# Optimization experiments

Measured on AMD Instinct MI355X. Metric: run time of the kernel, lower is better.

Reference implementation:

```python
import jax, jax.numpy as jnp
import numpy as np

B, S, H = 2, 2048, 1024
NH = 16
HD = H // NH
SCALE = 1.0 / np.sqrt(HD).astype(np.float32)


def setup_inputs() -> dict:
    key = jax.random.key(0)
    ks = jax.random.split(key, 7)
    lim = 1.0 / np.sqrt(H)  # lecun-ish init scale for linear weights
    return {
        "query": jax.random.normal(ks[0], (B, S, H), dtype=jnp.float32),
        "key_in": jax.random.normal(ks[1], (B, S, H), dtype=jnp.float32),
        "value": jax.random.normal(ks[2], (B, S, H), dtype=jnp.float32),
        "attention_mask": jnp.ones((B, S), dtype=jnp.int32),
        "Wq": jax.random.uniform(ks[3], (H, H), jnp.float32, -lim, lim),
        "Wk": jax.random.uniform(ks[4], (H, H), jnp.float32, -lim, lim),
        "Wv": jax.random.uniform(ks[5], (H, H), jnp.float32, -lim, lim),
        "Wo": jax.random.uniform(ks[6], (H, H), jnp.float32, -lim, lim),
    }


def reference(query, key_in, value, attention_mask, Wq, Wk, Wv, Wo):
    b, s, _ = query.shape
    # projections (no bias)
    q = (query @ Wq).reshape(b, s, NH, HD).transpose(0, 2, 1, 3)  # [b,h,s,d]
    k = (key_in @ Wk).reshape(b, s, NH, HD).transpose(0, 2, 1, 3)
    v = (value @ Wv).reshape(b, s, NH, HD).transpose(0, 2, 1, 3)

    scores = jnp.einsum("bhqd,bhkd->bhqk", q, k) * SCALE  # [b,h,s,s]
    mask = attention_mask[:, None, None, :]  # broadcast over heads & query pos
    scores = jnp.where(mask == 0, -1e9, scores)
    attn = jax.nn.softmax(scores, axis=-1)

    ctx = jnp.einsum("bhqk,bhkd->bhqd", attn, v)
    ctx = ctx.transpose(0, 2, 1, 3).reshape(b, s, H)
    out = ctx @ Wo
    return out, jnp.mean(attn, axis=1)
```

## Files before the change

kernel.cpp:

```cpp
#include <hip/hip_runtime.h>
#include <stdint.h>

#define BB 2
#define SS 2048
#define HH 1024
#define NHEAD 16
#define HDIM 64

constexpr int   BSROWS = BB * SS;
constexpr float SCALE  = 0.125f;
constexpr float LOG2E  = 1.4426950408889634f;
constexpr float SL     = SCALE * LOG2E;

typedef __bf16 bf16;
typedef __attribute__((ext_vector_type(8))) __bf16 bf16x8;
typedef __attribute__((ext_vector_type(4))) __bf16 bf16x4;
typedef __attribute__((ext_vector_type(4))) float  f32x4;

#define MFMA16(a, b, c) __builtin_amdgcn_mfma_f32_16x16x32_bf16((a), (b), (c), 0, 0, 0)

__device__ __forceinline__ void gload_lds16(const void* g, void* l) {
  __builtin_amdgcn_global_load_lds((const __attribute__((address_space(1))) void*)g,
                                   (__attribute__((address_space(3))) void*)l, 16, 0, 0);
}

__global__ __launch_bounds__(256) void cvt_in(const float* __restrict__ q, const float* __restrict__ k,
                                              const float* __restrict__ v, const int* __restrict__ mask,
                                              bf16* __restrict__ xq, bf16* __restrict__ xk,
                                              bf16* __restrict__ xv, float* __restrict__ bias2) {
  int i = blockIdx.x * 256 + threadIdx.x;
  int e = i * 4;
  f32x4 a = *(const f32x4*)(q + e);
  f32x4 b = *(const f32x4*)(k + e);
  f32x4 c = *(const f32x4*)(v + e);
  *(bf16x4*)(xq + e) = __builtin_convertvector(a, bf16x4);
  *(bf16x4*)(xk + e) = __builtin_convertvector(b, bf16x4);
  *(bf16x4*)(xv + e) = __builtin_convertvector(c, bf16x4);
  if (i < BB * SS) bias2[i] = mask[i] ? 0.0f : -1e9f * LOG2E;
}

__global__ __launch_bounds__(256) void cvt_wt(const float* __restrict__ Wq, const float* __restrict__ Wk,
                                              const float* __restrict__ Wv, const float* __restrict__ Wo,
                                              bf16* __restrict__ Wt) {
  __shared__ float tile[32][33];
  int z = blockIdx.z;
  const float* W = (z == 0) ? Wq : (z == 1) ? Wk : (z == 2) ? Wv : Wo;
  bf16* out = Wt + (size_t)z * HH * HH;
  int bx = blockIdx.x * 32, by = blockIdx.y * 32;
  int tx = threadIdx.x, ty = threadIdx.y;
#pragma unroll
  for (int j = 0; j < 32; j += 8)
    tile[ty + j][tx] = W[(size_t)(by + ty + j) * HH + bx + tx];
  __syncthreads();
#pragma unroll
  for (int j = 0; j < 32; j += 8)
    out[(size_t)(bx + ty + j) * HH + by + tx] = (bf16)tile[tx][ty + j];
}

__global__ __launch_bounds__(256) void gemm128(const bf16* __restrict__ Abase, const bf16* __restrict__ Btbase,
                                               bf16* __restrict__ Qo, bf16* __restrict__ Ko,
                                               bf16* __restrict__ Vto, float* __restrict__ outF, int mode) {
  int id  = blockIdx.x + 8 * blockIdx.y + 256 * blockIdx.z;
  int nwg = 256 * gridDim.z;
  int sw  = (id & 7) * (nwg >> 3) + (id >> 3);
  int bx  = sw & 7, by = (sw >> 3) & 31, bz = sw >> 8;

  int zmode = (mode < 0) ? bz : mode;
  const bf16* A  = Abase  + (mode < 0 ? (size_t)bz * BSROWS * HH : 0);
  const bf16* Bt = Btbase + (mode < 0 ? (size_t)bz * HH * HH : 0);

  __shared__ __align__(16) bf16 lA[128 * 32];
  __shared__ __align__(16) bf16 lB[128 * 32];

  int t = threadIdx.x;
  int w = t >> 6, l = t & 63, lg = l >> 4, lr = l & 15;
  int m0 = by * 128, n0 = bx * 128;
  int wr = (w >> 1) * 64, wc = (w & 1) * 64;

  f32x4 zero4 = {0.f, 0.f, 0.f, 0.f};
  f32x4 acc[4][4];
#pragma unroll
  for (int i = 0; i < 4; i++)
#pragma unroll
    for (int j = 0; j < 4; j++) acc[i][j] = zero4;

  for (int k0 = 0; k0 < HH; k0 += 32) {
#pragma unroll
    for (int i = 0; i < 2; i++) {
      int idx = i * 256 + t;
      gload_lds16(A  + (size_t)(m0 + (idx >> 2)) * HH + k0 + (idx & 3) * 8, &lA[(i * 256 + w * 64) * 8]);
      gload_lds16(Bt + (size_t)(n0 + (idx >> 2)) * HH + k0 + (idx & 3) * 8, &lB[(i * 256 + w * 64) * 8]);
    }
    __syncthreads();
    bf16x8 af[4], bq[4];
#pragma unroll
    for (int mi = 0; mi < 4; mi++) af[mi] = *(const bf16x8*)&lA[(wr + mi * 16 + lr) * 32 + lg * 8];
#pragma unroll
    for (int ni = 0; ni < 4; ni++) bq[ni] = *(const bf16x8*)&lB[(wc + ni * 16 + lr) * 32 + lg * 8];
#pragma unroll
    for (int mi = 0; mi < 4; mi++)
#pragma unroll
      for (int ni = 0; ni < 4; ni++)
        acc[mi][ni] = MFMA16(af[mi], bq[ni], acc[mi][ni]);
    __syncthreads();
  }

#pragma unroll
  for (int mi = 0; mi < 4; mi++) {
    int row0 = m0 + wr + mi * 16 + lg * 4;
#pragma unroll
    for (int ni = 0; ni < 4; ni++) {
      int col = n0 + wc + ni * 16 + lr;
      if (zmode == 3) {
#pragma unroll
        for (int r = 0; r < 4; r++) outF[(size_t)(row0 + r) * HH + col] = acc[mi][ni][r];
      } else if (zmode == 2) {
        int b = row0 >> 11, s0 = row0 & (SS - 1);
        int h = col >> 6, d = col & 63;
        bf16x4 pk;
#pragma unroll
        for (int r = 0; r < 4; r++) pk[r] = (bf16)acc[mi][ni][r];
        *(bf16x4*)&Vto[((size_t)(b * NHEAD + h) * HDIM + d) * SS + s0] = pk;
      } else {
        bf16* dst = (zmode == 0) ? Qo : Ko;
        int h = col >> 6, d = col & 63;
#pragma unroll
        for (int r = 0; r < 4; r++) {
          int row = row0 + r;
          int b = row >> 11, s = row & (SS - 1);
          dst[((size_t)(b * NHEAD + h) * SS + s) * HDIM + d] = (bf16)acc[mi][ni][r];
        }
      }
    }
  }
}

__global__ __launch_bounds__(256, 2) void attn_pv(const bf16* __restrict__ Q, const bf16* __restrict__ K,
                                                  const bf16* __restrict__ Vt, const float* __restrict__ bias2,
                                                  float* __restrict__ invl, bf16* __restrict__ ctx) {
  int id = blockIdx.x + 16 * blockIdx.y + 256 * blockIdx.z;
  int sw = (id & 7) * 64 + (id >> 3);
  int b = sw >> 8, h = (sw >> 4) & 15, q0 = (sw & 15) * 128;
  int t = threadIdx.x, w = t >> 6, l = t & 63, lg = l >> 4, lr = l & 15;
  size_t hb = ((size_t)b * NHEAD + h) * SS;
  const bf16* Qh = Q + hb * HDIM;
  const bf16* Kh = K + hb * HDIM;
  const bf16* Vh = Vt + ((size_t)b * NHEAD + h) * HDIM * SS;
  const float* biasb = bias2 + b * SS;

  __shared__ __align__(16) bf16 sK[64][72];
  __shared__ __align__(16) bf16 sV[64][72];
  __shared__ __align__(16) bf16 lp[4][32][72];

  int r0 = t >> 3, c0 = (t & 7) * 8;
  bf16x8 kreg[2], vreg[2];

  int qa = q0 + w * 32;
  int rowa = qa + lr, rowb = qa + 16 + lr;
  bf16x8 qf0a = *(const bf16x8*)&Qh[(size_t)rowa * HDIM + lg * 8];
  bf16x8 qf1a = *(const bf16x8*)&Qh[(size_t)rowa * HDIM + 32 + lg * 8];
  bf16x8 qf0b = *(const bf16x8*)&Qh[(size_t)rowb * HDIM + lg * 8];
  bf16x8 qf1b = *(const bf16x8*)&Qh[(size_t)rowb * HDIM + 32 + lg * 8];

  f32x4 zero4 = {0.f, 0.f, 0.f, 0.f};
  f32x4 lacca = zero4, laccb = zero4;
  f32x4 ctxa[4], ctxb[4];
#pragma unroll
  for (int nd = 0; nd < 4; nd++) { ctxa[nd] = zero4; ctxb[nd] = zero4; }

#pragma unroll
  for (int i = 0; i < 2; i++) {
    int row = i * 32 + r0;
    kreg[i] = *(const bf16x8*)&Kh[(size_t)row * HDIM + c0];
    vreg[i] = *(const bf16x8*)&Vh[(size_t)row * SS + c0];
  }
#pragma unroll
  for (int i = 0; i < 2; i++) {
    int row = i * 32 + r0;
    *(bf16x8*)&sK[row][c0] = kreg[i];
    *(bf16x8*)&sV[row][c0] = vreg[i];
  }

  for (int kt = 0; kt < 32; kt++) {
    int k0 = kt * 64;
    __syncthreads();
    if (kt < 31) {
      int kn = k0 + 64;
#pragma unroll
      for (int i = 0; i < 2; i++) {
        int row = i * 32 + r0;
        kreg[i] = *(const bf16x8*)&Kh[(size_t)(kn + row) * HDIM + c0];
        vreg[i] = *(const bf16x8*)&Vh[(size_t)row * SS + kn + c0];
      }
    }
    f32x4 acca[4], accb[4];
#pragma unroll
    for (int ni = 0; ni < 4; ni++) {
      const bf16* kp = &sK[ni * 16 + lr][lg * 8];
      bf16x8 kf0 = *(const bf16x8*)kp;
      bf16x8 kf1 = *(const bf16x8*)(kp + 32);
      acca[ni] = MFMA16(kf1, qf1a, MFMA16(kf0, qf0a, zero4));
      accb[ni] = MFMA16(kf1, qf1b, MFMA16(kf0, qf0b, zero4));
    }
    f32x4 pa4[4], pb4[4];
#pragma unroll
    for (int ni = 0; ni < 4; ni++) {
      f32x4 bv = *(const f32x4*)&biasb[k0 + ni * 16 + lg * 4];
      f32x4 za = acca[ni] * SL + bv;
      f32x4 zb = accb[ni] * SL + bv;
#pragma unroll
      for (int r = 0; r < 4; r++) {
        pa4[ni][r] = __builtin_amdgcn_exp2f(za[r]);
        pb4[ni][r] = __builtin_amdgcn_exp2f(zb[r]);
      }
    }
    lacca += (pa4[0] + pa4[1]) + (pa4[2] + pa4[3]);
    laccb += (pb4[0] + pb4[1]) + (pb4[2] + pb4[3]);
#pragma unroll
    for (int ni = 0; ni < 4; ni++) {
      *(bf16x4*)&lp[w][lr][ni * 16 + lg * 4]      = __builtin_convertvector(pa4[ni], bf16x4);
      *(bf16x4*)&lp[w][16 + lr][ni * 16 + lg * 4] = __builtin_convertvector(pb4[ni], bf16x4);
    }
#pragma unroll
    for (int kk = 0; kk < 2; kk++) {
      bf16x8 paa = *(const bf16x8*)&lp[w][lr][kk * 32 + lg * 8];
      bf16x8 pab = *(const bf16x8*)&lp[w][16 + lr][kk * 32 + lg * 8];
#pragma unroll
      for (int nd = 0; nd < 4; nd++) {
        bf16x8 vf = *(const bf16x8*)&sV[nd * 16 + lr][kk * 32 + lg * 8];
        ctxa[nd] = MFMA16(paa, vf, ctxa[nd]);
        ctxb[nd] = MFMA16(pab, vf, ctxb[nd]);
      }
    }
    __syncthreads();
    if (kt < 31) {
#pragma unroll
      for (int i = 0; i < 2; i++) {
        int row = i * 32 + r0;
        *(bf16x8*)&sK[row][c0] = kreg[i];
        *(bf16x8*)&sV[row][c0] = vreg[i];
      }
    }
  }

  float lsa = (lacca[0] + lacca[1]) + (lacca[2] + lacca[3]);
  float lsb = (laccb[0] + laccb[1]) + (laccb[2] + laccb[3]);
  lsa += __shfl_xor(lsa, 16); lsa += __shfl_xor(lsa, 32);
  lsb += __shfl_xor(lsb, 16); lsb += __shfl_xor(lsb, 32);
  float ila = 1.0f / lsa, ilb = 1.0f / lsb;
  f32x4 ilva, ilvb;
#pragma unroll
  for (int r = 0; r < 4; r++) { ilva[r] = __shfl(ila, lg * 4 + r); ilvb[r] = __shfl(ilb, lg * 4 + r); }
#pragma unroll
  for (int nd = 0; nd < 4; nd++)
#pragma unroll
    for (int r = 0; r < 4; r++) {
      int ra = qa + lg * 4 + r, rb = qa + 16 + lg * 4 + r;
      ctx[(size_t)(b * SS + ra) * HH + h * HDIM + nd * 16 + lr] = (bf16)(ctxa[nd][r] * ilva[r]);
      ctx[(size_t)(b * SS + rb) * HH + h * HDIM + nd * 16 + lr] = (bf16)(ctxb[nd][r] * ilvb[r]);
    }
  if (l < 16) {
    invl[hb + qa + l]      = ila;
    invl[hb + qa + 16 + l] = ilb;
  }
}

__global__ __launch_bounds__(256, 4) void attn_mean(const bf16* __restrict__ Q, const bf16* __restrict__ K,
                                                    const float* __restrict__ bias2,
                                                    const float* __restrict__ invl, float* __restrict__ meanOut) {
  int id = blockIdx.x + 16 * blockIdx.y + 512 * blockIdx.z;
  int sw = (id & 7) * 128 + (id >> 3);
  int b = sw >> 9, kc0 = ((sw >> 4) & 31) * 64, q0 = (sw & 15) * 128;
  int t = threadIdx.x, w = t >> 6, l = t & 63, lg = l >> 4, lr = l & 15;
  const float* biasb = bias2 + b * SS;
  __shared__ __align__(16) bf16 sK[2][64][64];

  int rloc = l >> 3;
  int csw  = (l & 7) ^ (rloc & 7);
  int swz  = lr & 7;

  int qa = q0 + w * 32;
  int rowa = qa + lr, rowb = qa + 16 + lr;

  f32x4 bv[4];
#pragma unroll
  for (int ni = 0; ni < 4; ni++) bv[ni] = *(const f32x4*)&biasb[kc0 + ni * 16 + lg * 4];

  f32x4 zero4 = {0.f, 0.f, 0.f, 0.f};
  f32x4 macca[4], maccb[4];
#pragma unroll
  for (int ni = 0; ni < 4; ni++) { macca[ni] = zero4; maccb[ni] = zero4; }

  bf16x8 qf0a, qf1a, qf0b, qf1b;
  float ila, ilb;
  {
    const bf16* Kh0 = K + ((size_t)b * NHEAD) * SS * HDIM;
#pragma unroll
    for (int i = 0; i < 2; i++) {
      int rs = w * 16 + i * 8;
      gload_lds16(Kh0 + (size_t)(kc0 + rs + rloc) * HDIM + csw * 8, &sK[0][rs][0]);
    }
    const bf16* Qh0 = Q + ((size_t)b * NHEAD) * SS * HDIM;
    qf0a = *(const bf16x8*)&Qh0[(size_t)rowa * HDIM + lg * 8];
    qf1a = *(const bf16x8*)&Qh0[(size_t)rowa * HDIM + 32 + lg * 8];
    qf0b = *(const bf16x8*)&Qh0[(size_t)rowb * HDIM + lg * 8];
    qf1b = *(const bf16x8*)&Qh0[(size_t)rowb * HDIM + 32 + lg * 8];
    size_t hb0 = (size_t)b * NHEAD * SS;
    ila = invl[hb0 + rowa] * (1.0f / NHEAD);
    ilb = invl[hb0 + rowb] * (1.0f / NHEAD);
  }
  __syncthreads();

  for (int h = 0; h < NHEAD; h++) {
    int cur = h & 1;
    bf16x8 qn0a, qn1a, qn0b, qn1b;
    float ina = 0.f, inb = 0.f;
    if (h < NHEAD - 1) {
      size_t hbn = ((size_t)b * NHEAD + h + 1) * SS;
      const bf16* Khn = K + hbn * HDIM;
#pragma unroll
      for (int i = 0; i < 2; i++) {
        int rs = w * 16 + i * 8;
        gload_lds16(Khn + (size_t)(kc0 + rs + rloc) * HDIM + csw * 8, &sK[cur ^ 1][rs][0]);
      }
      const bf16* Qhn = Q + hbn * HDIM;
      qn0a = *(const bf16x8*)&Qhn[(size_t)rowa * HDIM + lg * 8];
      qn1a = *(const bf16x8*)&Qhn[(size_t)rowa * HDIM + 32 + lg * 8];
      qn0b = *(const bf16x8*)&Qhn[(size_t)rowb * HDIM + lg * 8];
      qn1b = *(const bf16x8*)&Qhn[(size_t)rowb * HDIM + 32 + lg * 8];
      ina = invl[hbn + rowa] * (1.0f / NHEAD);
      inb = invl[hbn + rowb] * (1.0f / NHEAD);
    }
#pragma unroll
    for (int ni = 0; ni < 4; ni++) {
      bf16x8 kf0 = *(const bf16x8*)&sK[cur][ni * 16 + lr][(lg ^ swz) * 8];
      bf16x8 kf1 = *(const bf16x8*)&sK[cur][ni * 16 + lr][((4 + lg) ^ swz) * 8];
      f32x4 acca = MFMA16(kf1, qf1a, MFMA16(kf0, qf0a, zero4));
      f32x4 accb = MFMA16(kf1, qf1b, MFMA16(kf0, qf0b, zero4));
      f32x4 za = acca * SL + bv[ni];
      f32x4 zb = accb * SL + bv[ni];
#pragma unroll
      for (int r = 0; r < 4; r++) {
        macca[ni][r] += __builtin_amdgcn_exp2f(za[r]) * ila;
        maccb[ni][r] += __builtin_amdgcn_exp2f(zb[r]) * ilb;
      }
    }
    if (h < NHEAD - 1) {
      qf0a = qn0a; qf1a = qn1a; qf0b = qn0b; qf1b = qn1b;
      ila = ina; ilb = inb;
      __syncthreads();
    }
  }
  float* meanB = meanOut + (size_t)b * SS * SS;
#pragma unroll
  for (int ni = 0; ni < 4; ni++) {
    *(f32x4*)&meanB[(size_t)rowa * SS + kc0 + ni * 16 + lg * 4] = macca[ni];
    *(f32x4*)&meanB[(size_t)rowb * SS + kc0 + ni * 16 + lg * 4] = maccb[ni];
  }
}

extern "C" void kernel_launch(void* const* d_in, const int* in_sizes, int n_in,
                              void* d_out, int out_size, void* d_ws, size_t ws_size,
                              hipStream_t stream) {
  const float* query  = (const float*)d_in[0];
  const float* key_in = (const float*)d_in[1];
  const float* value  = (const float*)d_in[2];
  const int*   mask   = (const int*)d_in[3];
  const float* Wq     = (const float*)d_in[4];
  const float* Wk     = (const float*)d_in[5];
  const float* Wv     = (const float*)d_in[6];
  const float* Wo     = (const float*)d_in[7];

  char* ws = (char*)d_ws;
  bf16*  Xb    = (bf16*)(ws);
  bf16*  Wt    = (bf16*)(ws + 25165824);
  bf16*  Qb    = (bf16*)(ws + 33554432);
  bf16*  Kb    = (bf16*)(ws + 41943040);
  bf16*  Vtb   = (bf16*)(ws + 50331648);
  float* invlb = (float*)(ws + 58982400);
  float* biasb = (float*)(ws + 59244544);
  bf16*  ctxb  = Xb;

  float* outF  = (float*)d_out;
  float* meanF = outF + (size_t)BB * SS * HH;

  cvt_in<<<4096, 256, 0, stream>>>(query, key_in, value, mask,
                                   Xb, Xb + 4194304, Xb + 8388608, biasb);
  cvt_wt<<<dim3(32, 32, 4), dim3(32, 8), 0, stream>>>(Wq, Wk, Wv, Wo, Wt);
  gemm128<<<dim3(8, 32, 3), 256, 0, stream>>>(Xb, Wt, Qb, Kb, Vtb, nullptr, -1);
  attn_pv<<<dim3(16, 16, 2), 256, 0, stream>>>(Qb, Kb, Vtb, biasb, invlb, ctxb);
  attn_mean<<<dim3(16, 32, 2), 256, 0, stream>>>(Qb, Kb, biasb, invlb, meanF);
  gemm128<<<dim3(8, 32, 1), 256, 0, stream>>>(ctxb, Wt + 3 * (size_t)HH * HH,
                                              nullptr, nullptr, nullptr, outF, 3);
}
```

Baseline: 192.5 us.

## Double-buffer LDS tiles in projection GEMM and attention kernels

Both the GEMM and the attention-PV kernel now use two LDS buffers for their operand tiles. The next K-tile's global loads are issued into the alternate buffer while the current buffer is consumed by MFMAs. In the attention kernel this removes one of the two barriers per key tile. It doubles LDS use, which could reduce occupancy.

```diff
diff --git a/kernel.cpp b/kernel.cpp
--- a/kernel.cpp
+++ b/kernel.cpp
@@ -69,8 +69,8 @@
   const bf16* A  = Abase  + (mode < 0 ? (size_t)bz * BSROWS * HH : 0);
   const bf16* Bt = Btbase + (mode < 0 ? (size_t)bz * HH * HH : 0);
 
-  __shared__ __align__(16) bf16 lA[128 * 32];
-  __shared__ __align__(16) bf16 lB[128 * 32];
+  __shared__ __align__(16) bf16 lA[2][128 * 32];
+  __shared__ __align__(16) bf16 lB[2][128 * 32];
 
   int t = threadIdx.x;
   int w = t >> 6, l = t & 63, lg = l >> 4, lr = l & 15;
@@ -84,19 +84,30 @@
 #pragma unroll
     for (int j = 0; j < 4; j++) acc[i][j] = zero4;
 
-  for (int k0 = 0; k0 < HH; k0 += 32) {
-#pragma unroll
-    for (int i = 0; i < 2; i++) {
-      int idx = i * 256 + t;
-      gload_lds16(A  + (size_t)(m0 + (idx >> 2)) * HH + k0 + (idx & 3) * 8, &lA[(i * 256 + w * 64) * 8]);
-      gload_lds16(Bt + (size_t)(n0 + (idx >> 2)) * HH + k0 + (idx & 3) * 8, &lB[(i * 256 + w * 64) * 8]);
-    }
-    __syncthreads();
+#pragma unroll
+  for (int i = 0; i < 2; i++) {
+    int idx = i * 256 + t;
+    gload_lds16(A  + (size_t)(m0 + (idx >> 2)) * HH + (idx & 3) * 8, &lA[0][(i * 256 + w * 64) * 8]);
+    gload_lds16(Bt + (size_t)(n0 + (idx >> 2)) * HH + (idx & 3) * 8, &lB[0][(i * 256 + w * 64) * 8]);
+  }
+  __syncthreads();
+
+  for (int kt = 0; kt < 32; kt++) {
+    int cur = kt & 1;
+    if (kt < 31) {
+      int kn = (kt + 1) * 32;
+#pragma unroll
+      for (int i = 0; i < 2; i++) {
+        int idx = i * 256 + t;
+        gload_lds16(A  + (size_t)(m0 + (idx >> 2)) * HH + kn + (idx & 3) * 8, &lA[cur ^ 1][(i * 256 + w * 64) * 8]);
+        gload_lds16(Bt + (size_t)(n0 + (idx >> 2)) * HH + kn + (idx & 3) * 8, &lB[cur ^ 1][(i * 256 + w * 64) * 8]);
+      }
+    }
     bf16x8 af[4], bq[4];
 #pragma unroll
-    for (int mi = 0; mi < 4; mi++) af[mi] = *(const bf16x8*)&lA[(wr + mi * 16 + lr) * 32 + lg * 8];
-#pragma unroll
-    for (int ni = 0; ni < 4; ni++) bq[ni] = *(const bf16x8*)&lB[(wc + ni * 16 + lr) * 32 + lg * 8];
+    for (int mi = 0; mi < 4; mi++) af[mi] = *(const bf16x8*)&lA[cur][(wr + mi * 16 + lr) * 32 + lg * 8];
+#pragma unroll
+    for (int ni = 0; ni < 4; ni++) bq[ni] = *(const bf16x8*)&lB[cur][(wc + ni * 16 + lr) * 32 + lg * 8];
 #pragma unroll
     for (int mi = 0; mi < 4; mi++)
 #pragma unroll
@@ -148,8 +159,8 @@
   const bf16* Vh = Vt + ((size_t)b * NHEAD + h) * HDIM * SS;
   const float* biasb = bias2 + b * SS;
 
-  __shared__ __align__(16) bf16 sK[64][72];
-  __shared__ __align__(16) bf16 sV[64][72];
+  __shared__ __align__(16) bf16 sK[2][64][72];
+  __shared__ __align__(16) bf16 sV[2][64][72];
   __shared__ __align__(16) bf16 lp[4][32][72];
 
   int r0 = t >> 3, c0 = (t & 7) * 8;
@@ -177,13 +188,13 @@
 #pragma unroll
   for (int i = 0; i < 2; i++) {
     int row = i * 32 + r0;
-    *(bf16x8*)&sK[row][c0] = kreg[i];
-    *(bf16x8*)&sV[row][c0] = vreg[i];
-  }
+    *(bf16x8*)&sK[0][row][c0] = kreg[i];
+    *(bf16x8*)&sV[0][row][c0] = vreg[i];
+  }
+  __syncthreads();
 
   for (int kt = 0; kt < 32; kt++) {
-    int k0 = kt * 64;
-    __syncthreads();
+    int k0 = kt * 64, cur = kt & 1;
     if (kt < 31) {
       int kn = k0 + 64;
 #pragma unroll
@@ -196,7 +207,7 @@
     f32x4 acca[4], accb[4];
 #pragma unroll
     for (int ni = 0; ni < 4; ni++) {
-      const bf16* kp = &sK[ni * 16 + lr][lg * 8];
+      const bf16* kp = &sK[cur][ni * 16 + lr][lg * 8];
       bf16x8 kf0 = *(const bf16x8*)kp;
       bf16x8 kf1 = *(const bf16x8*)(kp + 32);
       acca[ni] = MFMA16(kf1, qf1a, MFMA16(kf0, qf0a, zero4));
@@ -227,19 +238,19 @@
       bf16x8 pab = *(const bf16x8*)&lp[w][16 + lr][kk * 32 + lg * 8];
 #pragma unroll
       for (int nd = 0; nd < 4; nd++) {
-        bf16x8 vf = *(const bf16x8*)&sV[nd * 16 + lr][kk * 32 + lg * 8];
+        bf16x8 vf = *(const bf16x8*)&sV[cur][nd * 16 + lr][kk * 32 + lg * 8];
         ctxa[nd] = MFMA16(paa, vf, ctxa[nd]);
         ctxb[nd] = MFMA16(pab, vf, ctxb[nd]);
       }
     }
-    __syncthreads();
     if (kt < 31) {
 #pragma unroll
       for (int i = 0; i < 2; i++) {
         int row = i * 32 + r0;
-        *(bf16x8*)&sK[row][c0] = kreg[i];
-        *(bf16x8*)&sV[row][c0] = vreg[i];
-      }
+        *(bf16x8*)&sK[cur ^ 1][row][c0] = kreg[i];
+        *(bf16x8*)&sV[cur ^ 1][row][c0] = vreg[i];
+      }
+      __syncthreads();
     }
   }
 
```

Result: faster. 180.3 us (-6.4%).
